# Kernel optimization log

Hardware: AMD Instinct MI355X
Metric: run time of the kernel (lower is better)

## Reference

```python
import jax, jax.numpy as jnp
import numpy as np

K = 5        # kernel_size per pseudo-dim
DIM = 2      # pseudo-coordinate dimensionality
K2 = K * K   # total kernel weight matrices
N_NODES = 50000


def spline_basis(edge_attr):
    """Open B-spline basis, degree=1, dim=2. Returns basis [E,4], weight_index [E,4]."""
    v = edge_attr * (K - 1)                      # [E,2], pseudo in [0,1]
    lo = jnp.floor(v)
    frac = v - lo                                # [E,2]
    lo = lo.astype(jnp.int32)
    fac = jnp.stack([1.0 - frac, frac], axis=-1)                 # [E,2,2] (dim, bit)
    idx = jnp.clip(lo[..., None] + jnp.arange(2), 0, K - 1)      # [E,2,2]
    b0 = jnp.array([0, 1, 0, 1])  # bit for dim 0, per spline term
    b1 = jnp.array([0, 0, 1, 1])  # bit for dim 1
    basis = fac[:, 0, b0] * fac[:, 1, b1]        # [E,4]
    wi = idx[:, 0, b0] * K + idx[:, 1, b1]       # [E,4] flat kernel index
    return basis, wi


def spline_conv(x, src, dst, basis, wi, W, root, bias, n_nodes):
    """SplineConv with mean aggregation, root weight and bias.
    x:[N,Fin] W:[K2,Fin,Fout] root:[Fin,Fout] bias:[Fout]"""
    E = src.shape[0]
    K2_, Fin, Fout = W.shape
    # scatter the 4 sparse basis values into a dense per-edge kernel-coeff matrix [E,K2]
    coeff = jnp.zeros((E, K2_), x.dtype).at[jnp.arange(E)[:, None], wi].add(basis)
    xj = x[src]                                  # gather source features [E,Fin]
    msg = jnp.zeros((E, Fout), x.dtype)
    for k in range(K2_):                         # fixed small loop over 25 kernels
        msg = msg + coeff[:, k:k + 1] * (xj @ W[k])
    agg = jax.ops.segment_sum(msg, dst, num_segments=n_nodes)    # [N,Fout]
    deg = jax.ops.segment_sum(jnp.ones((E,), x.dtype), dst, num_segments=n_nodes)
    agg = agg / jnp.clip(deg, 1.0)[:, None]      # mean aggregation
    return agg + x @ root + bias


def setup_inputs() -> dict:
    key = jax.random.key(0)
    ks = jax.random.split(key, 9)
    E = 800000
    Fin, H, C = 64, 16, 7
    x = jax.random.normal(ks[0], (N_NODES, Fin), dtype=jnp.float32)
    edge_index = jax.random.randint(ks[1], (2, E), 0, N_NODES, dtype=jnp.int64)
    edge_attr = jax.random.uniform(ks[2], (E, DIM), dtype=jnp.float32)
    s1 = 1.0 / np.sqrt(Fin)
    s2 = 1.0 / np.sqrt(H)
    W1 = jax.random.uniform(ks[3], (K2, Fin, H), jnp.float32, -s1, s1)
    root1 = jax.random.uniform(ks[4], (Fin, H), jnp.float32, -s1, s1)
    bias1 = jax.random.uniform(ks[5], (H,), jnp.float32, -s1, s1)
    W2 = jax.random.uniform(ks[6], (K2, H, C), jnp.float32, -s2, s2)
    root2 = jax.random.uniform(ks[7], (H, C), jnp.float32, -s2, s2)
    bias2 = jax.random.uniform(ks[8], (C,), jnp.float32, -s2, s2)
    return {"x": x, "edge_index": edge_index, "edge_attr": edge_attr,
            "W1": W1, "root1": root1, "bias1": bias1,
            "W2": W2, "root2": root2, "bias2": bias2}


def reference(x, edge_index, edge_attr, W1, root1, bias1, W2, root2, bias2):
    src = edge_index[0]
    dst = edge_index[1]
    basis, wi = spline_basis(edge_attr)
    h = jax.nn.relu(spline_conv(x, src, dst, basis, wi, W1, root1, bias1, N_NODES))
    # dropout(p=0.6) is identity in eval mode
    out = spline_conv(h, src, dst, basis, wi, W2, root2, bias2, N_NODES)
    return jax.nn.log_softmax(out, axis=1)
```

## Files before the change

kernel.cpp:

```cpp
#include <hip/hip_runtime.h>

#define KK2 25
#define FIN 64
#define HH 16
#define CC 7
#define KSPLIT 5

#define SCAN_VPT 4
#define SCAN_BLK 256
#define SCAN_CHUNK (SCAN_VPT * SCAN_BLK)

__device__ inline unsigned short f2bf(float f) {
    unsigned u = __float_as_uint(f);
    return (unsigned short)((u + 0x7FFFu + ((u >> 16) & 1u)) >> 16);
}
__device__ inline float bf2f(unsigned short b) {
    return __uint_as_float(((unsigned)b) << 16);
}

__global__ void k_hist(const int* __restrict__ ei, int* __restrict__ cnt, int E) {
    int e = blockIdx.x * 256 + threadIdx.x;
    if (e < E) atomicAdd(&cnt[ei[E + e]], 1);
}

__global__ void k_bsum(const int* __restrict__ cnt, int* __restrict__ bsum, int N) {
    int b = blockIdx.x, t = threadIdx.x;
    int base = b * SCAN_CHUNK + t * SCAN_VPT;
    int s = 0;
#pragma unroll
    for (int j = 0; j < SCAN_VPT; j++) {
        int i = base + j;
        if (i < N) s += cnt[i];
    }
#pragma unroll
    for (int d = 1; d < 64; d <<= 1) s += __shfl_xor(s, d, 64);
    __shared__ int sd[SCAN_BLK / 64];
    if ((t & 63) == 0) sd[t >> 6] = s;
    __syncthreads();
    if (t == 0) {
        int tot = 0;
        for (int w = 0; w < SCAN_BLK / 64; w++) tot += sd[w];
        bsum[b] = tot;
    }
}

__global__ void k_bscan(const int* __restrict__ bsum, int* __restrict__ boff, int nblk) {
    int t = threadIdx.x;
    __shared__ int sd[256];
    int v = (t < nblk) ? bsum[t] : 0;
    sd[t] = v;
    __syncthreads();
    for (int off = 1; off < 256; off <<= 1) {
        int u = (t >= off) ? sd[t - off] : 0;
        __syncthreads();
        sd[t] += u;
        __syncthreads();
    }
    boff[t] = sd[t] - v;
}

__global__ void k_sfin(const int* __restrict__ cnt, const int* __restrict__ boff,
                       int* __restrict__ rowStart, int* __restrict__ cursor, int N) {
    int b = blockIdx.x, t = threadIdx.x;
    int base = b * SCAN_CHUNK + t * SCAN_VPT;
    int v[SCAN_VPT];
    int s = 0;
#pragma unroll
    for (int j = 0; j < SCAN_VPT; j++) {
        int i = base + j;
        v[j] = (i < N) ? cnt[i] : 0;
        s += v[j];
    }
    __shared__ int sd[SCAN_BLK];
    sd[t] = s;
    __syncthreads();
    for (int off = 1; off < SCAN_BLK; off <<= 1) {
        int u = (t >= off) ? sd[t - off] : 0;
        __syncthreads();
        sd[t] += u;
        __syncthreads();
    }
    int run = sd[t] - s + boff[b];
#pragma unroll
    for (int j = 0; j < SCAN_VPT; j++) {
        int i = base + j;
        if (i < N) {
            rowStart[i] = run;
            cursor[i] = run;
            run += v[j];
            if (i == N - 1) rowStart[N] = run;
        }
    }
}

__global__ void k_scatter(const float* __restrict__ attr, const int* __restrict__ ei,
                          int* __restrict__ cursor, uint4* __restrict__ rec, int E) {
    int e = blockIdx.x * 256 + threadIdx.x;
    if (e >= E) return;
    float v0 = attr[2 * e] * 4.0f, v1 = attr[2 * e + 1] * 4.0f;
    float l0 = floorf(v0), l1 = floorf(v1);
    float f0 = v0 - l0, f1 = v1 - l1;
    int i0 = (int)l0, i1 = (int)l1;
    int i0a = min(max(i0, 0), 4), i0b = min(max(i0 + 1, 0), 4);
    int i1a = min(max(i1, 0), 4), i1b = min(max(i1 + 1, 0), 4);
    float bx = (1.0f - f0) * (1.0f - f1);
    float by = f0 * (1.0f - f1);
    float bz = (1.0f - f0) * f1;
    float bw = f0 * f1;
    unsigned pack = (unsigned)(i0a * 5 + i1a) | ((unsigned)(i0b * 5 + i1a) << 8) |
                    ((unsigned)(i0a * 5 + i1b) << 16) | ((unsigned)(i0b * 5 + i1b) << 24);
    int s = ei[e], d = ei[E + e];
    int pos = atomicAdd(&cursor[d], 1);
    uint4 r;
    r.x = (unsigned)f2bf(bx) | ((unsigned)f2bf(by) << 16);
    r.y = (unsigned)f2bf(bz) | ((unsigned)f2bf(bw) << 16);
    r.z = (unsigned)s;
    r.w = pack;
    rec[pos] = r;
}

__global__ void k_prepW(const float* __restrict__ W1, const float* __restrict__ W2,
                        float* __restrict__ B1t, float* __restrict__ W2p) {
    int tid = blockIdx.x * 256 + threadIdx.x;
    if (tid < KK2 * FIN * HH) {
        int c = tid >> 6, i = tid & 63;
        int k = c >> 4, h = c & 15;
        B1t[tid] = W1[(k * FIN + i) * HH + h];
    }
    if (tid < KK2 * HH * 8) {
        int k = tid >> 7, r = tid & 127;
        int i = r >> 3, c = r & 7;
        W2p[tid] = (c < CC) ? W2[(k * HH + i) * CC + c] : 0.0f;
    }
}

__global__ void k_y1(const float* __restrict__ x, const float* __restrict__ B1t,
                     unsigned short* __restrict__ y1Tb, int N, int nbl) {
    __shared__ uint4 sh[4][144];
    int kg = blockIdx.x / nbl;
    int nwin = blockIdx.x % nbl;
    int n = nwin * 256 + threadIdx.x;
    int wv = threadIdx.x >> 6, lane = threadIdx.x & 63;
    bool active = (n < N);
    float4 xr[16];
    if (active) {
        const float4* xp = (const float4*)(x + (size_t)n * 64);
#pragma unroll
        for (int i = 0; i < 16; i++) xr[i] = xp[i];
    }
    int nwb = nwin * 256 + wv * 64;
    int valid = min(64, max(0, N - nwb)) * 2;

    for (int dk = 0; dk < KSPLIT; dk++) {
        int k = kg * KSPLIT + dk;
        const float* B = B1t + k * 16 * 64;
        unsigned tmp[8];
        if (active) {
#pragma unroll
            for (int h4 = 0; h4 < 4; h4++) {
                float a0 = 0, a1 = 0, a2 = 0, a3 = 0;
                const float4* b0 = (const float4*)(B + (h4 * 4 + 0) * 64);
                const float4* b1 = (const float4*)(B + (h4 * 4 + 1) * 64);
                const float4* b2 = (const float4*)(B + (h4 * 4 + 2) * 64);
                const float4* b3 = (const float4*)(B + (h4 * 4 + 3) * 64);
#pragma unroll
                for (int i = 0; i < 16; i++) {
                    float4 xi = xr[i];
                    float4 v0 = b0[i], v1 = b1[i], v2 = b2[i], v3 = b3[i];
                    a0 += xi.x * v0.x + xi.y * v0.y + xi.z * v0.z + xi.w * v0.w;
                    a1 += xi.x * v1.x + xi.y * v1.y + xi.z * v1.z + xi.w * v1.w;
                    a2 += xi.x * v2.x + xi.y * v2.y + xi.z * v2.z + xi.w * v2.w;
                    a3 += xi.x * v3.x + xi.y * v3.y + xi.z * v3.z + xi.w * v3.w;
                }
                tmp[h4 * 2 + 0] = (unsigned)f2bf(a0) | ((unsigned)f2bf(a1) << 16);
                tmp[h4 * 2 + 1] = (unsigned)f2bf(a2) | ((unsigned)f2bf(a3) << 16);
            }
        } else {
#pragma unroll
            for (int j = 0; j < 8; j++) tmp[j] = 0;
        }
        int i0 = lane * 2, i1 = lane * 2 + 1;
        sh[wv][i0 + (i0 >> 3)] = make_uint4(tmp[0], tmp[1], tmp[2], tmp[3]);
        sh[wv][i1 + (i1 >> 3)] = make_uint4(tmp[4], tmp[5], tmp[6], tmp[7]);
        __syncthreads();
        uint4* gbase = (uint4*)(y1Tb + ((size_t)k * N + nwb) * 16);
        int j0 = lane, j1 = lane + 64;
        if (j0 < valid) gbase[j0] = sh[wv][j0 + (j0 >> 3)];
        if (j1 < valid) gbase[j1] = sh[wv][j1 + (j1 >> 3)];
        __syncthreads();
    }
}

__global__ void k_agg1u(const int* __restrict__ rowStart, const uint4* __restrict__ rec,
                        const unsigned short* __restrict__ y1Tb, const float* __restrict__ x,
                        const float* __restrict__ root1, const float* __restrict__ bias1,
                        float* __restrict__ h1, int N) {
    int n = blockIdx.x * 4 + (threadIdx.x >> 6);
    if (n >= N) return;
    int lane = threadIdx.x & 63;
    int sub = lane >> 4, h = lane & 15;
    int start = rowStart[n], end = rowStart[n + 1];
    float acc = 0.0f;
    size_t NN = (size_t)N;
    for (int i = start + sub; i < end; i += 4) {
        uint4 r = rec[i];
        float bx = bf2f((unsigned short)(r.x & 0xffffu));
        float by = bf2f((unsigned short)(r.x >> 16));
        float bz = bf2f((unsigned short)(r.y & 0xffffu));
        float bw = bf2f((unsigned short)(r.y >> 16));
        int s = (int)r.z;
        unsigned w = r.w;
        acc += bx * bf2f(y1Tb[((w & 255u) * NN + s) * 16 + h]);
        acc += by * bf2f(y1Tb[(((w >> 8) & 255u) * NN + s) * 16 + h]);
        acc += bz * bf2f(y1Tb[(((w >> 16) & 255u) * NN + s) * 16 + h]);
        acc += bw * bf2f(y1Tb[((w >> 24) * NN + s) * 16 + h]);
    }
    acc += __shfl_xor(acc, 16, 64);
    acc += __shfl_xor(acc, 32, 64);
    float inv = 1.0f / (float)max(end - start, 1);
    float rv = acc * inv + bias1[h];
    const float* xrow = x + (size_t)n * 64;
#pragma unroll 8
    for (int i = 0; i < 64; i++) rv += xrow[i] * root1[i * 16 + h];
    rv = fmaxf(rv, 0.0f);
    if (lane < 16) h1[(size_t)n * 16 + h] = rv;
}

__global__ void k_y2(const float* __restrict__ h1, const float* __restrict__ W2p,
                     unsigned short* __restrict__ y2Tb, int N, int nbl) {
    int kg = blockIdx.x / nbl;
    int n = (blockIdx.x % nbl) * 256 + threadIdx.x;
    if (n >= N) return;
    float hreg[16];
    const float4* hp = (const float4*)(h1 + (size_t)n * 16);
#pragma unroll
    for (int j = 0; j < 4; j++) {
        float4 v = hp[j];
        hreg[4 * j] = v.x; hreg[4 * j + 1] = v.y;
        hreg[4 * j + 2] = v.z; hreg[4 * j + 3] = v.w;
    }
#pragma unroll
    for (int dk = 0; dk < KSPLIT; dk++) {
        int k = kg * KSPLIT + dk;
        float z[8] = {0, 0, 0, 0, 0, 0, 0, 0};
        const float4* wp = (const float4*)(W2p + k * 128);
#pragma unroll
        for (int i = 0; i < 16; i++) {
            float hi = hreg[i];
            float4 lo = wp[2 * i], hv = wp[2 * i + 1];
            z[0] += hi * lo.x; z[1] += hi * lo.y; z[2] += hi * lo.z; z[3] += hi * lo.w;
            z[4] += hi * hv.x; z[5] += hi * hv.y; z[6] += hi * hv.z; z[7] += hi * hv.w;
        }
        uint4 p;
        p.x = (unsigned)f2bf(z[0]) | ((unsigned)f2bf(z[1]) << 16);
        p.y = (unsigned)f2bf(z[2]) | ((unsigned)f2bf(z[3]) << 16);
        p.z = (unsigned)f2bf(z[4]) | ((unsigned)f2bf(z[5]) << 16);
        p.w = (unsigned)f2bf(z[6]) | ((unsigned)f2bf(z[7]) << 16);
        *(uint4*)(y2Tb + ((size_t)k * N + n) * 8) = p;
    }
}

__global__ void k_agg2f(const int* __restrict__ rowStart, const uint4* __restrict__ rec,
                        const unsigned short* __restrict__ y2Tb, const float* __restrict__ h1,
                        const float* __restrict__ root2, const float* __restrict__ bias2,
                        float* __restrict__ out, int N) {
    int n = blockIdx.x * 4 + (threadIdx.x >> 6);
    if (n >= N) return;
    int lane = threadIdx.x & 63;
    int sub = lane >> 3, c = lane & 7;
    int start = rowStart[n], end = rowStart[n + 1];
    float acc = 0.0f;
    size_t NN = (size_t)N;
    for (int i = start + sub; i < end; i += 8) {
        uint4 r = rec[i];
        float bx = bf2f((unsigned short)(r.x & 0xffffu));
        float by = bf2f((unsigned short)(r.x >> 16));
        float bz = bf2f((unsigned short)(r.y & 0xffffu));
        float bw = bf2f((unsigned short)(r.y >> 16));
        int s = (int)r.z;
        unsigned w = r.w;
        acc += bx * bf2f(y2Tb[((w & 255u) * NN + s) * 8 + c]);
        acc += by * bf2f(y2Tb[(((w >> 8) & 255u) * NN + s) * 8 + c]);
        acc += bz * bf2f(y2Tb[(((w >> 16) & 255u) * NN + s) * 8 + c]);
        acc += bw * bf2f(y2Tb[((w >> 24) * NN + s) * 8 + c]);
    }
    acc += __shfl_xor(acc, 8, 64);
    acc += __shfl_xor(acc, 16, 64);
    acc += __shfl_xor(acc, 32, 64);
    float inv = 1.0f / (float)max(end - start, 1);
    float z;
    if (c < CC) {
        z = acc * inv + bias2[c];
        const float* hrow = h1 + (size_t)n * 16;
#pragma unroll
        for (int i = 0; i < 16; i++) z += hrow[i] * root2[i * CC + c];
    } else {
        z = -1e30f;
    }
    float m = z;
    m = fmaxf(m, __shfl_xor(m, 1, 64));
    m = fmaxf(m, __shfl_xor(m, 2, 64));
    m = fmaxf(m, __shfl_xor(m, 4, 64));
    float ex = (c < CC) ? expf(z - m) : 0.0f;
    float ssum = ex;
    ssum += __shfl_xor(ssum, 1, 64);
    ssum += __shfl_xor(ssum, 2, 64);
    ssum += __shfl_xor(ssum, 4, 64);
    float ls = logf(ssum);
    if (lane < CC) out[(size_t)n * 7 + c] = z - m - ls;
}

extern "C" void kernel_launch(void* const* d_in, const int* in_sizes, int n_in,
                              void* d_out, int out_size, void* d_ws, size_t ws_size,
                              hipStream_t stream) {
    const float* x     = (const float*)d_in[0];
    const int*   ei    = (const int*)d_in[1];
    const float* attr  = (const float*)d_in[2];
    const float* W1    = (const float*)d_in[3];
    const float* root1 = (const float*)d_in[4];
    const float* bias1 = (const float*)d_in[5];
    const float* W2    = (const float*)d_in[6];
    const float* root2 = (const float*)d_in[7];
    const float* bias2 = (const float*)d_in[8];
    float* out = (float*)d_out;

    int N = in_sizes[0] / FIN;
    int E = in_sizes[1] / 2;

    char* w = (char*)d_ws;
    size_t off = 0;
    auto alloc = [&](size_t bytes) -> void* {
        void* p = w + off;
        off += (bytes + 255) & ~(size_t)255;
        return p;
    };
    int*      cnt      = (int*)alloc((size_t)N * 4);
    int*      rowStart = (int*)alloc((size_t)(N + 1) * 4);
    int*      cursor   = (int*)alloc((size_t)N * 4);
    int*      bsum     = (int*)alloc(260 * 4);
    int*      boff     = (int*)alloc(260 * 4);
    uint4*    rec      = (uint4*)alloc((size_t)E * 16);
    float*    h1       = (float*)alloc((size_t)N * 64);
    float*    B1t      = (float*)alloc((size_t)KK2 * FIN * HH * 4);
    float*    W2p      = (float*)alloc((size_t)KK2 * HH * 8 * 4);
    unsigned short* y1Tb = (unsigned short*)alloc((size_t)N * 400 * 2);
    unsigned short* y2Tb = y1Tb;
    (void)ws_size; (void)n_in; (void)out_size;

    hipMemsetAsync(cnt, 0, (size_t)N * 4, stream);

    int ebl = (E + 255) / 256;
    int nbl = (N + 255) / 256;
    int sblk = (N + SCAN_CHUNK - 1) / SCAN_CHUNK;

    k_hist<<<ebl, 256, 0, stream>>>(ei, cnt, E);
    k_bsum<<<sblk, SCAN_BLK, 0, stream>>>(cnt, bsum, N);
    k_bscan<<<1, 256, 0, stream>>>(bsum, boff, sblk);
    k_sfin<<<sblk, SCAN_BLK, 0, stream>>>(cnt, boff, rowStart, cursor, N);
    k_scatter<<<ebl, 256, 0, stream>>>(attr, ei, cursor, rec, E);
    k_prepW<<<(KK2 * FIN * HH + 255) / 256, 256, 0, stream>>>(W1, W2, B1t, W2p);
    k_y1<<<KSPLIT * nbl, 256, 0, stream>>>(x, B1t, y1Tb, N, nbl);
    k_agg1u<<<(N + 3) / 4, 256, 0, stream>>>(rowStart, rec, y1Tb, x, root1, bias1, h1, N);
    k_y2<<<KSPLIT * nbl, 256, 0, stream>>>(h1, W2p, y2Tb, N, nbl);
    k_agg2f<<<(N + 3) / 4, 256, 0, stream>>>(rowStart, rec, y2Tb, h1, root2, bias2, out, N);
}
```

Measured before the change: 296.6 us.

## Fuse layer-2 kernel transform into edge aggregation, dropping y2 precompute

Removes the k_y2 kernel that precomputed per-node, per-kernel transformed features (25×N×8 bf16) and the later scattered gathers from that table. Instead, the layer-2 aggregation gathers the 16-float h1 row of each source node and multiplies it on the fly by a transposed W2 layout held in cache, for each of the 4 spline terms. This trades a full kernel launch and a large intermediate write/read for extra per-edge FLOPs (4×16 MACs per lane per edge) and repeated h1 row loads across the 8 channel lanes. It also keeps the layer-2 messages in fp32 instead of bf16.

```diff
diff --git a/kernel.cpp b/kernel.cpp
--- a/kernel.cpp
+++ b/kernel.cpp
@@ -120,17 +120,17 @@
 }
 
 __global__ void k_prepW(const float* __restrict__ W1, const float* __restrict__ W2,
-                        float* __restrict__ B1t, float* __restrict__ W2p) {
+                        float* __restrict__ B1t, float* __restrict__ W2t) {
     int tid = blockIdx.x * 256 + threadIdx.x;
     if (tid < KK2 * FIN * HH) {
         int c = tid >> 6, i = tid & 63;
         int k = c >> 4, h = c & 15;
         B1t[tid] = W1[(k * FIN + i) * HH + h];
     }
-    if (tid < KK2 * HH * 8) {
+    if (tid < KK2 * 8 * HH) {
         int k = tid >> 7, r = tid & 127;
-        int i = r >> 3, c = r & 7;
-        W2p[tid] = (c < CC) ? W2[(k * HH + i) * CC + c] : 0.0f;
+        int c = r >> 4, i = r & 15;
+        W2t[tid] = (c < CC) ? W2[(k * HH + i) * CC + c] : 0.0f;
     }
 }
 
@@ -226,42 +226,8 @@
     if (lane < 16) h1[(size_t)n * 16 + h] = rv;
 }
 
-__global__ void k_y2(const float* __restrict__ h1, const float* __restrict__ W2p,
-                     unsigned short* __restrict__ y2Tb, int N, int nbl) {
-    int kg = blockIdx.x / nbl;
-    int n = (blockIdx.x % nbl) * 256 + threadIdx.x;
-    if (n >= N) return;
-    float hreg[16];
-    const float4* hp = (const float4*)(h1 + (size_t)n * 16);
-#pragma unroll
-    for (int j = 0; j < 4; j++) {
-        float4 v = hp[j];
-        hreg[4 * j] = v.x; hreg[4 * j + 1] = v.y;
-        hreg[4 * j + 2] = v.z; hreg[4 * j + 3] = v.w;
-    }
-#pragma unroll
-    for (int dk = 0; dk < KSPLIT; dk++) {
-        int k = kg * KSPLIT + dk;
-        float z[8] = {0, 0, 0, 0, 0, 0, 0, 0};
-        const float4* wp = (const float4*)(W2p + k * 128);
-#pragma unroll
-        for (int i = 0; i < 16; i++) {
-            float hi = hreg[i];
-            float4 lo = wp[2 * i], hv = wp[2 * i + 1];
-            z[0] += hi * lo.x; z[1] += hi * lo.y; z[2] += hi * lo.z; z[3] += hi * lo.w;
-            z[4] += hi * hv.x; z[5] += hi * hv.y; z[6] += hi * hv.z; z[7] += hi * hv.w;
-        }
-        uint4 p;
-        p.x = (unsigned)f2bf(z[0]) | ((unsigned)f2bf(z[1]) << 16);
-        p.y = (unsigned)f2bf(z[2]) | ((unsigned)f2bf(z[3]) << 16);
-        p.z = (unsigned)f2bf(z[4]) | ((unsigned)f2bf(z[5]) << 16);
-        p.w = (unsigned)f2bf(z[6]) | ((unsigned)f2bf(z[7]) << 16);
-        *(uint4*)(y2Tb + ((size_t)k * N + n) * 8) = p;
-    }
-}
-
-__global__ void k_agg2f(const int* __restrict__ rowStart, const uint4* __restrict__ rec,
-                        const unsigned short* __restrict__ y2Tb, const float* __restrict__ h1,
+__global__ void k_agg2d(const int* __restrict__ rowStart, const uint4* __restrict__ rec,
+                        const float* __restrict__ h1, const float* __restrict__ W2t,
                         const float* __restrict__ root2, const float* __restrict__ bias2,
                         float* __restrict__ out, int N) {
     int n = blockIdx.x * 4 + (threadIdx.x >> 6);
@@ -270,19 +236,28 @@
     int sub = lane >> 3, c = lane & 7;
     int start = rowStart[n], end = rowStart[n + 1];
     float acc = 0.0f;
-    size_t NN = (size_t)N;
     for (int i = start + sub; i < end; i += 8) {
         uint4 r = rec[i];
-        float bx = bf2f((unsigned short)(r.x & 0xffffu));
-        float by = bf2f((unsigned short)(r.x >> 16));
-        float bz = bf2f((unsigned short)(r.y & 0xffffu));
-        float bw = bf2f((unsigned short)(r.y >> 16));
+        float bt0 = bf2f((unsigned short)(r.x & 0xffffu));
+        float bt1 = bf2f((unsigned short)(r.x >> 16));
+        float bt2 = bf2f((unsigned short)(r.y & 0xffffu));
+        float bt3 = bf2f((unsigned short)(r.y >> 16));
         int s = (int)r.z;
         unsigned w = r.w;
-        acc += bx * bf2f(y2Tb[((w & 255u) * NN + s) * 8 + c]);
-        acc += by * bf2f(y2Tb[(((w >> 8) & 255u) * NN + s) * 8 + c]);
-        acc += bz * bf2f(y2Tb[(((w >> 16) & 255u) * NN + s) * 8 + c]);
-        acc += bw * bf2f(y2Tb[((w >> 24) * NN + s) * 8 + c]);
+        const float4* hp = (const float4*)(h1 + (size_t)s * 16);
+        float4 h0 = hp[0], h1v = hp[1], h2 = hp[2], h3 = hp[3];
+        float bts[4] = {bt0, bt1, bt2, bt3};
+#pragma unroll
+        for (int t = 0; t < 4; t++) {
+            int wv = (int)((w >> (8 * t)) & 255u);
+            const float4* wp = (const float4*)(W2t + ((size_t)(wv * 8 + c)) * 16);
+            float4 a0 = wp[0], a1 = wp[1], a2 = wp[2], a3 = wp[3];
+            float m = h0.x * a0.x + h0.y * a0.y + h0.z * a0.z + h0.w * a0.w
+                    + h1v.x * a1.x + h1v.y * a1.y + h1v.z * a1.z + h1v.w * a1.w
+                    + h2.x * a2.x + h2.y * a2.y + h2.z * a2.z + h2.w * a2.w
+                    + h3.x * a3.x + h3.y * a3.y + h3.z * a3.z + h3.w * a3.w;
+            acc += bts[t] * m;
+        }
     }
     acc += __shfl_xor(acc, 8, 64);
     acc += __shfl_xor(acc, 16, 64);
@@ -342,9 +317,8 @@
     uint4*    rec      = (uint4*)alloc((size_t)E * 16);
     float*    h1       = (float*)alloc((size_t)N * 64);
     float*    B1t      = (float*)alloc((size_t)KK2 * FIN * HH * 4);
-    float*    W2p      = (float*)alloc((size_t)KK2 * HH * 8 * 4);
+    float*    W2t      = (float*)alloc((size_t)KK2 * 8 * HH * 4);
     unsigned short* y1Tb = (unsigned short*)alloc((size_t)N * 400 * 2);
-    unsigned short* y2Tb = y1Tb;
     (void)ws_size; (void)n_in; (void)out_size;
 
     hipMemsetAsync(cnt, 0, (size_t)N * 4, stream);
@@ -358,9 +332,8 @@
     k_bscan<<<1, 256, 0, stream>>>(bsum, boff, sblk);
     k_sfin<<<sblk, SCAN_BLK, 0, stream>>>(cnt, boff, rowStart, cursor, N);
     k_scatter<<<ebl, 256, 0, stream>>>(attr, ei, cursor, rec, E);
-    k_prepW<<<(KK2 * FIN * HH + 255) / 256, 256, 0, stream>>>(W1, W2, B1t, W2p);
+    k_prepW<<<(KK2 * FIN * HH + 255) / 256, 256, 0, stream>>>(W1, W2, B1t, W2t);
     k_y1<<<KSPLIT * nbl, 256, 0, stream>>>(x, B1t, y1Tb, N, nbl);
     k_agg1u<<<(N + 3) / 4, 256, 0, stream>>>(rowStart, rec, y1Tb, x, root1, bias1, h1, N);
-    k_y2<<<KSPLIT * nbl, 256, 0, stream>>>(h1, W2p, y2Tb, N, nbl);
-    k_agg2f<<<(N + 3) / 4, 256, 0, stream>>>(rowStart, rec, y2Tb, h1, root2, bias2, out, N);
-}
+    k_agg2d<<<(N + 3) / 4, 256, 0, stream>>>(rowStart, rec, h1, W2t, root2, bias2, out, N);
+}
```

Result: slower. 364.5 us (+22.9%).

## Store adjacent spline kernel pairs contiguously to halve gather rows in aggregation

Applied to the files above, without the earlier changes.

The layer-1 projected features are now stored as pairs (k, k+1) per node, 32 bf16 values per row, so each edge in the first aggregation touches two 64-byte rows instead of four 32-byte rows. The edge record keeps only two packed kernel indices, and the second aggregation recomputes the other two indices from them. This aims to cut scattered memory transactions in the gather-heavy aggregation. The cost is a larger intermediate buffer with duplicated data, which adds write traffic in k_y1 and a double-buffered shared-memory staging step there.

```diff
diff --git a/kernel.cpp b/kernel.cpp
--- a/kernel.cpp
+++ b/kernel.cpp
@@ -4,7 +4,6 @@
 #define FIN 64
 #define HH 16
 #define CC 7
-#define KSPLIT 5
 
 #define SCAN_VPT 4
 #define SCAN_BLK 256
@@ -102,20 +101,20 @@
     float f0 = v0 - l0, f1 = v1 - l1;
     int i0 = (int)l0, i1 = (int)l1;
     int i0a = min(max(i0, 0), 4), i0b = min(max(i0 + 1, 0), 4);
-    int i1a = min(max(i1, 0), 4), i1b = min(max(i1 + 1, 0), 4);
+    int i1a = min(max(i1, 0), 4);
     float bx = (1.0f - f0) * (1.0f - f1);
     float by = f0 * (1.0f - f1);
     float bz = (1.0f - f0) * f1;
     float bw = f0 * f1;
-    unsigned pack = (unsigned)(i0a * 5 + i1a) | ((unsigned)(i0b * 5 + i1a) << 8) |
-                    ((unsigned)(i0a * 5 + i1b) << 16) | ((unsigned)(i0b * 5 + i1b) << 24);
+    unsigned pA = (unsigned)(i0a * 5 + i1a);
+    unsigned pB = (unsigned)(i0b * 5 + i1a);
     int s = ei[e], d = ei[E + e];
     int pos = atomicAdd(&cursor[d], 1);
     uint4 r;
     r.x = (unsigned)f2bf(bx) | ((unsigned)f2bf(by) << 16);
     r.y = (unsigned)f2bf(bz) | ((unsigned)f2bf(bw) << 16);
     r.z = (unsigned)s;
-    r.w = pack;
+    r.w = pA | (pB << 8);
     rec[pos] = r;
 }
 
@@ -135,9 +134,9 @@
 }
 
 __global__ void k_y1(const float* __restrict__ x, const float* __restrict__ B1t,
-                     unsigned short* __restrict__ y1Tb, int N, int nbl) {
-    __shared__ uint4 sh[4][144];
-    int kg = blockIdx.x / nbl;
+                     unsigned short* __restrict__ y1q, int N, int nbl) {
+    __shared__ uint4 sh[4][2][144];
+    int i0 = blockIdx.x / nbl;
     int nwin = blockIdx.x % nbl;
     int n = nwin * 256 + threadIdx.x;
     int wv = threadIdx.x >> 6, lane = threadIdx.x & 63;
@@ -149,10 +148,11 @@
         for (int i = 0; i < 16; i++) xr[i] = xp[i];
     }
     int nwb = nwin * 256 + wv * 64;
-    int valid = min(64, max(0, N - nwb)) * 2;
-
-    for (int dk = 0; dk < KSPLIT; dk++) {
-        int k = kg * KSPLIT + dk;
+    int validf = min(64, max(0, N - nwb)) * 4;
+    size_t NN = (size_t)N;
+
+    for (int i1 = 0; i1 < 5; i1++) {
+        int k = i0 * 5 + i1;
         const float* B = B1t + k * 16 * 64;
         unsigned tmp[8];
         if (active) {
@@ -179,20 +179,44 @@
 #pragma unroll
             for (int j = 0; j < 8; j++) tmp[j] = 0;
         }
-        int i0 = lane * 2, i1 = lane * 2 + 1;
-        sh[wv][i0 + (i0 >> 3)] = make_uint4(tmp[0], tmp[1], tmp[2], tmp[3]);
-        sh[wv][i1 + (i1 >> 3)] = make_uint4(tmp[4], tmp[5], tmp[6], tmp[7]);
-        __syncthreads();
-        uint4* gbase = (uint4*)(y1Tb + ((size_t)k * N + nwb) * 16);
-        int j0 = lane, j1 = lane + 64;
-        if (j0 < valid) gbase[j0] = sh[wv][j0 + (j0 >> 3)];
-        if (j1 < valid) gbase[j1] = sh[wv][j1 + (j1 >> 3)];
+        int slot = i1 & 1;
+        int i0e = lane * 2, i1e = lane * 2 + 1;
+        sh[wv][slot][i0e + (i0e >> 3)] = make_uint4(tmp[0], tmp[1], tmp[2], tmp[3]);
+        sh[wv][slot][i1e + (i1e >> 3)] = make_uint4(tmp[4], tmp[5], tmp[6], tmp[7]);
+        __syncthreads();
+        if (i1 >= 1) {
+            int p = i0 * 5 + (i1 - 1);
+            uint4* g4 = (uint4*)(y1q + ((size_t)p * NN + nwb) * 32);
+#pragma unroll
+            for (int j = 0; j < 4; j++) {
+                int f = j * 64 + lane;
+                if (f < validf) {
+                    int node = f >> 2, piece = f & 3;
+                    int idx = node * 2 + (piece & 1);
+                    int ss = (piece < 2) ? (slot ^ 1) : slot;
+                    g4[f] = sh[wv][ss][idx + (idx >> 3)];
+                }
+            }
+        }
+        if (i1 == 4) {
+            int p = i0 * 5 + 4;
+            uint4* g4 = (uint4*)(y1q + ((size_t)p * NN + nwb) * 32);
+#pragma unroll
+            for (int j = 0; j < 4; j++) {
+                int f = j * 64 + lane;
+                if (f < validf) {
+                    int node = f >> 2, piece = f & 3;
+                    int idx = node * 2 + (piece & 1);
+                    g4[f] = sh[wv][slot][idx + (idx >> 3)];
+                }
+            }
+        }
         __syncthreads();
     }
 }
 
 __global__ void k_agg1u(const int* __restrict__ rowStart, const uint4* __restrict__ rec,
-                        const unsigned short* __restrict__ y1Tb, const float* __restrict__ x,
+                        const unsigned short* __restrict__ y1q, const float* __restrict__ x,
                         const float* __restrict__ root1, const float* __restrict__ bias1,
                         float* __restrict__ h1, int N) {
     int n = blockIdx.x * 4 + (threadIdx.x >> 6);
@@ -210,10 +234,10 @@
         float bw = bf2f((unsigned short)(r.y >> 16));
         int s = (int)r.z;
         unsigned w = r.w;
-        acc += bx * bf2f(y1Tb[((w & 255u) * NN + s) * 16 + h]);
-        acc += by * bf2f(y1Tb[(((w >> 8) & 255u) * NN + s) * 16 + h]);
-        acc += bz * bf2f(y1Tb[(((w >> 16) & 255u) * NN + s) * 16 + h]);
-        acc += bw * bf2f(y1Tb[((w >> 24) * NN + s) * 16 + h]);
+        const unsigned short* rA = y1q + ((w & 255u) * NN + s) * 32;
+        const unsigned short* rB = y1q + (((w >> 8) & 255u) * NN + s) * 32;
+        acc += bx * bf2f(rA[h]) + bz * bf2f(rA[16 + h]);
+        acc += by * bf2f(rB[h]) + bw * bf2f(rB[16 + h]);
     }
     acc += __shfl_xor(acc, 16, 64);
     acc += __shfl_xor(acc, 32, 64);
@@ -240,8 +264,8 @@
         hreg[4 * j + 2] = v.z; hreg[4 * j + 3] = v.w;
     }
 #pragma unroll
-    for (int dk = 0; dk < KSPLIT; dk++) {
-        int k = kg * KSPLIT + dk;
+    for (int dk = 0; dk < 5; dk++) {
+        int k = kg * 5 + dk;
         float z[8] = {0, 0, 0, 0, 0, 0, 0, 0};
         const float4* wp = (const float4*)(W2p + k * 128);
 #pragma unroll
@@ -278,11 +302,13 @@
         float bz = bf2f((unsigned short)(r.y & 0xffffu));
         float bw = bf2f((unsigned short)(r.y >> 16));
         int s = (int)r.z;
-        unsigned w = r.w;
-        acc += bx * bf2f(y2Tb[((w & 255u) * NN + s) * 8 + c]);
-        acc += by * bf2f(y2Tb[(((w >> 8) & 255u) * NN + s) * 8 + c]);
-        acc += bz * bf2f(y2Tb[(((w >> 16) & 255u) * NN + s) * 8 + c]);
-        acc += bw * bf2f(y2Tb[((w >> 24) * NN + s) * 8 + c]);
+        unsigned pA = r.w & 255u, pB = (r.w >> 8) & 255u;
+        unsigned i1a = pA % 5u;
+        unsigned d = (i1a < 4u) ? 1u : 0u;
+        acc += bx * bf2f(y2Tb[(pA * NN + s) * 8 + c]);
+        acc += by * bf2f(y2Tb[(pB * NN + s) * 8 + c]);
+        acc += bz * bf2f(y2Tb[((pA + d) * NN + s) * 8 + c]);
+        acc += bw * bf2f(y2Tb[((pB + d) * NN + s) * 8 + c]);
     }
     acc += __shfl_xor(acc, 8, 64);
     acc += __shfl_xor(acc, 16, 64);
@@ -343,8 +369,8 @@
     float*    h1       = (float*)alloc((size_t)N * 64);
     float*    B1t      = (float*)alloc((size_t)KK2 * FIN * HH * 4);
     float*    W2p      = (float*)alloc((size_t)KK2 * HH * 8 * 4);
-    unsigned short* y1Tb = (unsigned short*)alloc((size_t)N * 400 * 2);
-    unsigned short* y2Tb = y1Tb;
+    unsigned short* y1q  = (unsigned short*)alloc((size_t)KK2 * N * 32 * 2);
+    unsigned short* y2Tb = y1q;
     (void)ws_size; (void)n_in; (void)out_size;
 
     hipMemsetAsync(cnt, 0, (size_t)N * 4, stream);
@@ -359,8 +385,8 @@
     k_sfin<<<sblk, SCAN_BLK, 0, stream>>>(cnt, boff, rowStart, cursor, N);
     k_scatter<<<ebl, 256, 0, stream>>>(attr, ei, cursor, rec, E);
     k_prepW<<<(KK2 * FIN * HH + 255) / 256, 256, 0, stream>>>(W1, W2, B1t, W2p);
-    k_y1<<<KSPLIT * nbl, 256, 0, stream>>>(x, B1t, y1Tb, N, nbl);
-    k_agg1u<<<(N + 3) / 4, 256, 0, stream>>>(rowStart, rec, y1Tb, x, root1, bias1, h1, N);
-    k_y2<<<KSPLIT * nbl, 256, 0, stream>>>(h1, W2p, y2Tb, N, nbl);
+    k_y1<<<5 * nbl, 256, 0, stream>>>(x, B1t, y1q, N, nbl);
+    k_agg1u<<<(N + 3) / 4, 256, 0, stream>>>(rowStart, rec, y1q, x, root1, bias1, h1, N);
+    k_y2<<<5 * nbl, 256, 0, stream>>>(h1, W2p, y2Tb, N, nbl);
     k_agg2f<<<(N + 3) / 4, 256, 0, stream>>>(rowStart, rec, y2Tb, h1, root2, bias2, out, N);
 }
```

Result: faster. 289.2 us (-2.5%).
